# Performance work log

Hardware: AMD Instinct MI355X
Metric: run time of the kernel (lower is better)

## Reference

```python
import jax, jax.numpy as jnp
import numpy as np

D = 768       # model dim
H = 8         # heads
DH = 96       # dim per head
M = 256       # FAVOR+ random features
DEPTH = 6
B = 8
NM = 4        # n_masks
FF = 3072     # 4*dim feedforward
N = 512       # tokens = (1024/16)*(128/16)


def setup_inputs() -> dict:
    key = jax.random.key(0)
    ks = jax.random.split(key, 16)
    g = lambda k, shape: jax.random.normal(k, shape, jnp.float32) * 0.02
    return {
        "mel": jax.random.normal(ks[0], (B, 1, 1024, 128), jnp.float32),
        "patch_w": g(ks[1], (D, 1, 16, 16)),
        "patch_b": jnp.zeros((D,), jnp.float32),
        "pos_embed": g(ks[2], (1, N, D)),
        "proj": jax.random.normal(ks[3], (M, DH), jnp.float32),  # FAVOR+ projection (buffer, no grad)
        "ln1_s": jnp.ones((DEPTH, D)), "ln1_b": jnp.zeros((DEPTH, D)),
        "qkv_w": g(ks[4], (DEPTH, D, 3 * D)), "qkv_b": jnp.zeros((DEPTH, 3 * D)),
        "ao_w": g(ks[5], (DEPTH, D, D)), "ao_b": jnp.zeros((DEPTH, D)),
        "ln2_s": jnp.ones((DEPTH, D)), "ln2_b": jnp.zeros((DEPTH, D)),
        "ff1_w": g(ks[6], (DEPTH, D, FF)), "ff1_b": jnp.zeros((DEPTH, FF)),
        "ff2_w": g(ks[7], (DEPTH, FF, D)), "ff2_b": jnp.zeros((DEPTH, D)),
        "mask_w": g(ks[8], (D, NM)), "mask_b": jnp.zeros((NM,), jnp.float32),
    }


def _ln(x, s, b):
    mu = x.mean(-1, keepdims=True)
    v = ((x - mu) ** 2).mean(-1, keepdims=True)
    return (x - mu) / jnp.sqrt(v + 1e-5) * s + b


def _phi(x, proj, is_query):
    # FAVOR+ softmax-kernel feature map. x: (b,h,n,d), proj: (m,d)
    xd = x * (x.shape[-1] ** -0.25)            # d^{-1/4} data normalizer
    u = jnp.einsum('bhnd,md->bhnm', xd, proj)
    diag = 0.5 * jnp.sum(xd * xd, axis=-1, keepdims=True)
    stab = jnp.max(u, axis=-1, keepdims=True) if is_query else jnp.max(u)
    stab = jax.lax.stop_gradient(stab)          # matches .detach() in performer
    return (jnp.exp(u - diag - stab) + 1e-4) * (proj.shape[0] ** -0.5)


def reference(mel, patch_w, patch_b, pos_embed, proj, ln1_s, ln1_b, qkv_w, qkv_b,
              ao_w, ao_b, ln2_s, ln2_b, ff1_w, ff1_b, ff2_w, ff2_b, mask_w, mask_b):
    # --- frozen AudioMAE patch embed (+pos embed), under no_grad in torch ---
    x = jax.lax.conv_general_dilated(mel, patch_w, (16, 16), 'VALID',
                                     dimension_numbers=('NCHW', 'OIHW', 'NCHW'))  # (B,D,64,8)
    b = x.shape[0]
    x = x.reshape(b, D, -1).transpose(0, 2, 1) + patch_b  # (B,N,D)
    x = x + pos_embed
    x = jax.lax.stop_gradient(x)
    proj = jax.lax.stop_gradient(proj)

    def heads(t):
        return t.reshape(b, -1, H, DH).transpose(0, 2, 1, 3)  # (b,h,n,dh)

    for l in range(DEPTH):
        # --- FAVOR+ linear attention block ---
        h = _ln(x, ln1_s[l], ln1_b[l])
        qkv = h @ qkv_w[l] + qkv_b[l]
        q, k, v = (heads(t) for t in jnp.split(qkv, 3, axis=-1))
        pq = _phi(q, proj, True)
        pk = _phi(k, proj, False)
        ctx = jnp.einsum('bhnm,bhne->bhme', pk, v)       # (b,h,m,dh) linear-time kv summary
        out = jnp.einsum('bhnm,bhme->bhne', pq, ctx)
        den = jnp.einsum('bhnm,bhm->bhn', pq, pk.sum(axis=2))
        out = out / den[..., None]
        out = out.transpose(0, 2, 1, 3).reshape(b, -1, D)
        x = x + out @ ao_w[l] + ao_b[l]
        # --- feedforward block ---
        h = _ln(x, ln2_s[l], ln2_b[l])
        h = jax.nn.gelu(h @ ff1_w[l] + ff1_b[l], approximate=False)
        x = x + h @ ff2_w[l] + ff2_b[l]

    logits = x @ mask_w + mask_b              # (B,N,M)
    masks = jax.nn.sigmoid(logits)
    return masks.transpose(0, 2, 1)           # (B,M,N)
```

## Files before the change

kernel.cpp:

```cpp
#include <hip/hip_runtime.h>
#include <hip/hip_bf16.h>

typedef __bf16 bf16;
typedef __bf16 bf16x8 __attribute__((ext_vector_type(8)));
typedef float f32x4 __attribute__((ext_vector_type(4)));
typedef unsigned int u32;

#define PHI_SCALE  0.31947154f
#define DIAG_SCALE 0.05103104f
#define FEAT_SCALE 0.0625f

__device__ __forceinline__ void glds16(const bf16* g, bf16* l) {
  __builtin_amdgcn_global_load_lds(
      (const __attribute__((address_space(1))) u32*)g,
      (__attribute__((address_space(3))) u32*)l, 16, 0, 0);
}

__device__ __forceinline__ void xcd_remap(int& bx, int& by) {
  int nbx = gridDim.x, nby = gridDim.y;
  int lin = bx + nbx * by;
  int xcd = lin & 7, idx = lin >> 3;
  int mloc = nbx >> 2, nloc = nby >> 1;
  int xm = xcd & 3, xn = xcd >> 2;
  bx = xm * mloc + (idx % mloc);
  by = xn * nloc + (idx / mloc);
}

__device__ __forceinline__ int swz_scol(int lane) {
  return (((lane & 3) ^ ((lane >> 3) & 3)) * 8);
}

__device__ __forceinline__ float waveSum(float v) {
#pragma unroll
  for (int o = 32; o > 0; o >>= 1) v += __shfl_xor(v, o, 64);
  return v;
}
__device__ __forceinline__ float waveMax(float v) {
#pragma unroll
  for (int o = 32; o > 0; o >>= 1) v = fmaxf(v, __shfl_xor(v, o, 64));
  return v;
}
__device__ __forceinline__ float blockSum(float v) {
  __shared__ float tmp[4];
  v = waveSum(v);
  if ((threadIdx.x & 63) == 0) tmp[threadIdx.x >> 6] = v;
  __syncthreads();
  float r = tmp[0] + tmp[1] + tmp[2] + tmp[3];
  __syncthreads();
  return r;
}
__device__ __forceinline__ float blockMax(float v) {
  __shared__ float tmp[4];
  v = waveMax(v);
  if ((threadIdx.x & 63) == 0) tmp[threadIdx.x >> 6] = v;
  __syncthreads();
  float r = fmaxf(fmaxf(tmp[0], tmp[1]), fmaxf(tmp[2], tmp[3]));
  __syncthreads();
  return r;
}

__global__ __launch_bounds__(256) void patches_kernel(const float* __restrict__ mel,
    bf16* __restrict__ patches) {
  int blk = blockIdx.x, t = threadIdx.x;
  int b = blk >> 9, n = blk & 511;
  int r0 = (n >> 3) << 4, c0 = (n & 7) << 4;
  patches[(size_t)blk * 256 + t] =
      (bf16)mel[((size_t)b * 1024 + r0 + (t >> 4)) * 128 + c0 + (t & 15)];
}

__global__ __launch_bounds__(256) void cvt_kernel(const float* __restrict__ src,
    bf16* __restrict__ dst, int n) {
  int i = blockIdx.x * 256 + threadIdx.x;
  if (i < n) dst[i] = (bf16)src[i];
}

__device__ __forceinline__ void tile_transpose(const float* __restrict__ src,
    bf16* __restrict__ dst, int K, int N, int bx, int by) {
  __shared__ float lds[64][65];
  int n0 = bx * 64, k0 = by * 64;
  int t = threadIdx.x;
  for (int idx = t; idx < 4096; idx += 256) {
    int r = idx >> 6, c = idx & 63;
    lds[r][c] = src[(size_t)(k0 + r) * N + n0 + c];
  }
  __syncthreads();
  for (int idx = t; idx < 4096; idx += 256) {
    int r = idx >> 6, c = idx & 63;
    dst[(size_t)(n0 + r) * K + k0 + c] = (bf16)lds[c][r];
  }
}
__global__ __launch_bounds__(256) void transpose4_kernel(
    const float* __restrict__ w0, bf16* __restrict__ d0,
    const float* __restrict__ w1, bf16* __restrict__ d1,
    const float* __restrict__ w2, bf16* __restrict__ d2,
    const float* __restrict__ w3, bf16* __restrict__ d3) {
  int i = blockIdx.x;
  if (i < 432)       { tile_transpose(w0, d0, 768, 2304, i % 36, i / 36); }
  else if (i < 576)  { i -= 432;  tile_transpose(w1, d1, 768, 768, i % 12, i / 12); }
  else if (i < 1152) { i -= 576;  tile_transpose(w2, d2, 768, 3072, i % 48, i / 48);}
  else               { i -= 1152; tile_transpose(w3, d3, 3072, 768, i % 12, i / 12);}
}

__global__ __launch_bounds__(256) void ln_kernel(float* __restrict__ x,
    const float* __restrict__ part,
    const float* __restrict__ s, const float* __restrict__ bta, bf16* __restrict__ h) {
  int row = blockIdx.x;
  float* xr = x + (size_t)row * 768;
  int t = threadIdx.x;
  float v0 = xr[t], v1 = xr[t + 256], v2 = xr[t + 512];
  if (part) {
    const float* p0 = part + (size_t)row * 768;
    const float* p1 = p0 + 4096ull * 768;
    v0 += p0[t]       + p1[t];
    v1 += p0[t + 256] + p1[t + 256];
    v2 += p0[t + 512] + p1[t + 512];
    xr[t] = v0; xr[t + 256] = v1; xr[t + 512] = v2;
  }
  float mu = blockSum(v0 + v1 + v2) * (1.f / 768.f);
  float d0 = v0 - mu, d1 = v1 - mu, d2 = v2 - mu;
  float var = blockSum(d0 * d0 + d1 * d1 + d2 * d2) * (1.f / 768.f);
  float inv = rsqrtf(var + 1e-5f);
  bf16* hr = h + (size_t)row * 768;
  hr[t]       = (bf16)(d0 * inv * s[t]       + bta[t]);
  hr[t + 256] = (bf16)(d1 * inv * s[t + 256] + bta[t + 256]);
  hr[t + 512] = (bf16)(d2 * inv * s[t + 512] + bta[t + 512]);
}

__global__ __launch_bounds__(256) void gemm128(const bf16* __restrict__ A,
    const bf16* __restrict__ B, const float* __restrict__ bias,
    bf16* __restrict__ outb, int N, int K, int mode) {
  __shared__ __attribute__((aligned(16))) bf16 lds_a[2 * 128 * 32];
  __shared__ __attribute__((aligned(16))) bf16 lds_b[2 * 128 * 32];
  int bx = blockIdx.x, by = blockIdx.y;
  xcd_remap(bx, by);
  const int t = threadIdx.x;
  const int m0 = bx * 128, n0 = by * 128;
  const int wave = t >> 6, lane = t & 63;
  const int quad = lane >> 4, id = lane & 15;
  const int wr = wave >> 1, wc = wave & 1;
  const int srow = lane >> 2, scol = swz_scol(lane);
  const bf16* pa0 = A + (size_t)(m0 + wave * 32 + srow) * K + scol;
  const bf16* pa1 = pa0 + (size_t)16 * K;
  const bf16* pb0 = B + (size_t)(n0 + wave * 32 + srow) * K + scol;
  const bf16* pb1 = pb0 + (size_t)16 * K;
  bf16* la = lds_a + wave * 1024;
  bf16* lb = lds_b + wave * 1024;
  const int sl = (quad ^ ((id >> 1) & 3)) * 8;
  f32x4 acc[4][4] = {};
  for (int k0 = 0; k0 < K; k0 += 64) {
    glds16(pa0, la);      glds16(pa1, la + 512);
    glds16(pa0 + 32, la + 4096); glds16(pa1 + 32, la + 4096 + 512);
    glds16(pb0, lb);      glds16(pb1, lb + 512);
    glds16(pb0 + 32, lb + 4096); glds16(pb1 + 32, lb + 4096 + 512);
    pa0 += 64; pa1 += 64; pb0 += 64; pb1 += 64;
    __syncthreads();
#pragma unroll
    for (int kh = 0; kh < 2; kh++) {
      bf16x8 af[4], bg[4];
#pragma unroll
      for (int i = 0; i < 4; i++)
        af[i] = *(bf16x8*)&lds_a[kh * 4096 + (wr * 64 + i * 16 + id) * 32 + sl];
#pragma unroll
      for (int j = 0; j < 4; j++)
        bg[j] = *(bf16x8*)&lds_b[kh * 4096 + (wc * 64 + j * 16 + id) * 32 + sl];
#pragma unroll
      for (int i = 0; i < 4; i++)
#pragma unroll
        for (int j = 0; j < 4; j++)
          acc[i][j] = __builtin_amdgcn_mfma_f32_16x16x32_bf16(af[i], bg[j], acc[i][j], 0, 0, 0);
    }
    __syncthreads();
  }
#pragma unroll
  for (int i = 0; i < 4; i++) {
#pragma unroll
    for (int j = 0; j < 4; j++) {
#pragma unroll
      for (int r = 0; r < 4; r++) {
        int rr = m0 + wr * 64 + i * 16 + quad * 4 + r;
        int cc = n0 + wc * 64 + j * 16 + id;
        float v = acc[i][j][r] + bias[cc];
        if (mode == 1) v = 0.5f * v * (1.0f + erff(v * 0.70710678f));
        outb[(size_t)rr * N + cc] = (bf16)v;
      }
    }
  }
}

__global__ __launch_bounds__(256) void gemm_b64(const bf16* __restrict__ A,
    const bf16* __restrict__ B, const float* __restrict__ bias,
    bf16* __restrict__ outb, float* __restrict__ xout,
    const float* __restrict__ pos, int N, int kchunk, int mode) {
  __shared__ __attribute__((aligned(16))) bf16 lds_a[2 * 128 * 32];
  __shared__ __attribute__((aligned(16))) bf16 lds_b[2 * 64 * 32];
  int bx = blockIdx.x, by = blockIdx.y;
  xcd_remap(bx, by);
  const int t = threadIdx.x;
  const int m0 = bx * 128, n0 = by * 64;
  const int kz = blockIdx.z;
  const int k_start = kz * kchunk;
  const int wave = t >> 6, lane = t & 63;
  const int quad = lane >> 4, id = lane & 15;
  const int srow = lane >> 2, scol = swz_scol(lane);
  const int K = kchunk * gridDim.z;
  const size_t slice = (size_t)kz * gridDim.x * 128 * N;
  const bf16* pa0 = A + (size_t)(m0 + wave * 32 + srow) * K + k_start + scol;
  const bf16* pa1 = pa0 + (size_t)16 * K;
  const bf16* pb  = B + (size_t)(n0 + wave * 16 + srow) * K + k_start + scol;
  bf16* la = lds_a + wave * 1024;
  bf16* lb = lds_b + wave * 512;
  const int sl = (quad ^ ((id >> 1) & 3)) * 8;
  f32x4 acc[2][4] = {};
  for (int k0 = 0; k0 < kchunk; k0 += 64) {
    glds16(pa0, la);      glds16(pa1, la + 512);
    glds16(pa0 + 32, la + 4096); glds16(pa1 + 32, la + 4096 + 512);
    glds16(pb, lb);       glds16(pb + 32, lb + 2048);
    pa0 += 64; pa1 += 64; pb += 64;
    __syncthreads();
#pragma unroll
    for (int kh = 0; kh < 2; kh++) {
      bf16x8 af[2], bg[4];
#pragma unroll
      for (int i = 0; i < 2; i++)
        af[i] = *(bf16x8*)&lds_a[kh * 4096 + (wave * 32 + i * 16 + id) * 32 + sl];
#pragma unroll
      for (int j = 0; j < 4; j++)
        bg[j] = *(bf16x8*)&lds_b[kh * 2048 + (j * 16 + id) * 32 + sl];
#pragma unroll
      for (int i = 0; i < 2; i++)
#pragma unroll
        for (int j = 0; j < 4; j++)
          acc[i][j] = __builtin_amdgcn_mfma_f32_16x16x32_bf16(af[i], bg[j], acc[i][j], 0, 0, 0);
    }
    __syncthreads();
  }
#pragma unroll
  for (int i = 0; i < 2; i++) {
#pragma unroll
    for (int j = 0; j < 4; j++) {
#pragma unroll
      for (int r = 0; r < 4; r++) {
        int rr = m0 + wave * 32 + i * 16 + quad * 4 + r;
        int cc = n0 + j * 16 + id;
        if (mode == 4) {
          float v = acc[i][j][r] + (kz == 0 ? bias[cc] : 0.f);
          xout[slice + (size_t)rr * N + cc] = v;
        } else {
          float v = acc[i][j][r] + bias[cc];
          if (mode == 0) {
            outb[(size_t)rr * N + cc] = (bf16)v;
          } else if (mode == 1) {
            outb[(size_t)rr * N + cc] = (bf16)(0.5f * v * (1.0f + erff(v * 0.70710678f)));
          } else {
            xout[(size_t)rr * N + cc] = v + pos[(size_t)(rr & 511) * 768 + cc];
          }
        }
      }
    }
  }
}

__global__ __launch_bounds__(256) void phi_q_kernel(const bf16* __restrict__ qkv,
    const bf16* __restrict__ proj, bf16* __restrict__ pq) {
  __shared__ __attribute__((aligned(16))) bf16 lA[3][64 * 32];
  __shared__ __attribute__((aligned(16))) bf16 lB[3][256 * 32];
  __shared__ float sqlds[64];
  const int t = threadIdx.x;
  const int nt = blockIdx.x, bh = blockIdx.y;
  const int b = bh >> 3, h = bh & 7;
  const int n0 = nt * 64;
  const bf16* Abase = qkv + ((size_t)(b * 512 + n0)) * 2304 + h * 96;
#pragma unroll
  for (int c = 0; c < 3; c++) {
    int v = c * 256 + t;
    int row = v / 12, s = v % 12;
    *(bf16x8*)&lA[s >> 2][row * 32 + (s & 3) * 8] = *(const bf16x8*)&Abase[(size_t)row * 2304 + s * 8];
  }
#pragma unroll
  for (int c = 0; c < 12; c++) {
    int v = c * 256 + t;
    int row = v / 12, s = v % 12;
    *(bf16x8*)&lB[s >> 2][row * 32 + (s & 3) * 8] = *(const bf16x8*)&proj[(size_t)row * 96 + s * 8];
  }
  __syncthreads();
  const int wave = t >> 6, lane = t & 63, quad = lane >> 4, id = lane & 15;
  f32x4 acc[16] = {};
  float sq = 0.f;
#pragma unroll
  for (int kb = 0; kb < 3; kb++) {
    bf16x8 af = *(bf16x8*)&lA[kb][(wave * 16 + id) * 32 + quad * 8];
#pragma unroll
    for (int e = 0; e < 8; e++) { float fv = (float)af[e]; sq += fv * fv; }
#pragma unroll
    for (int j = 0; j < 16; j++) {
      bf16x8 bg = *(bf16x8*)&lB[kb][(j * 16 + id) * 32 + quad * 8];
      acc[j] = __builtin_amdgcn_mfma_f32_16x16x32_bf16(af, bg, acc[j], 0, 0, 0);
    }
  }
  sq += __shfl_xor(sq, 16, 64);
  sq += __shfl_xor(sq, 32, 64);
  if (quad == 0) sqlds[wave * 16 + id] = sq;
  __syncthreads();
#pragma unroll
  for (int r = 0; r < 4; r++) {
    int rrow = quad * 4 + r;
    float dg = DIAG_SCALE * sqlds[wave * 16 + rrow];
    float mx = -1e30f;
#pragma unroll
    for (int j = 0; j < 16; j++) mx = fmaxf(mx, acc[j][r]);
    mx = fmaxf(mx, __shfl_xor(mx, 1, 64));
    mx = fmaxf(mx, __shfl_xor(mx, 2, 64));
    mx = fmaxf(mx, __shfl_xor(mx, 4, 64));
    mx = fmaxf(mx, __shfl_xor(mx, 8, 64));
    float umax = mx * PHI_SCALE;
#pragma unroll
    for (int j = 0; j < 16; j++) {
      float uu = acc[j][r] * PHI_SCALE;
      float val = (expf(uu - dg - umax) + 1e-4f) * FEAT_SCALE;
      pq[((size_t)bh * 512 + n0 + wave * 16 + rrow) * 256 + j * 16 + id] = (bf16)val;
    }
  }
}

__global__ __launch_bounds__(256) void phi_k_kernel(const bf16* __restrict__ qkv,
    const bf16* __restrict__ proj, bf16* __restrict__ pkT, float* __restrict__ kbm) {
  __shared__ __attribute__((aligned(16))) bf16 lA[3][64 * 32];
  __shared__ __attribute__((aligned(16))) bf16 lB[3][256 * 32];
  __shared__ float sqlds[64];
  __shared__ float bmax4[4];
  const int t = threadIdx.x;
  const int nt = blockIdx.x, bh = blockIdx.y;
  const int b = bh >> 3, h = bh & 7;
  const int n0 = nt * 64;
  const bf16* Abase = qkv + ((size_t)(b * 512 + n0)) * 2304 + 768 + h * 96;
#pragma unroll
  for (int c = 0; c < 3; c++) {
    int v = c * 256 + t;
    int row = v / 12, s = v % 12;
    *(bf16x8*)&lA[s >> 2][row * 32 + (s & 3) * 8] = *(const bf16x8*)&Abase[(size_t)row * 2304 + s * 8];
  }
#pragma unroll
  for (int c = 0; c < 12; c++) {
    int v = c * 256 + t;
    int row = v / 12, s = v % 12;
    *(bf16x8*)&lB[s >> 2][row * 32 + (s & 3) * 8] = *(const bf16x8*)&proj[(size_t)row * 96 + s * 8];
  }
  __syncthreads();
  const int wave = t >> 6, lane = t & 63, quad = lane >> 4, id = lane & 15;
  f32x4 acc[16] = {};
  float sq = 0.f;
#pragma unroll
  for (int kb = 0; kb < 3; kb++) {
    bf16x8 af = *(bf16x8*)&lA[kb][(wave * 16 + id) * 32 + quad * 8];
#pragma unroll
    for (int e = 0; e < 8; e++) { float fv = (float)af[e]; sq += fv * fv; }
#pragma unroll
    for (int j = 0; j < 16; j++) {
      bf16x8 bg = *(bf16x8*)&lB[kb][(j * 16 + id) * 32 + quad * 8];
      acc[j] = __builtin_amdgcn_mfma_f32_16x16x32_bf16(af, bg, acc[j], 0, 0, 0);
    }
  }
  sq += __shfl_xor(sq, 16, 64);
  sq += __shfl_xor(sq, 32, 64);
  if (quad == 0) sqlds[wave * 16 + id] = sq;
  float bm = -1e30f;
#pragma unroll
  for (int j = 0; j < 16; j++)
#pragma unroll
    for (int r = 0; r < 4; r++) bm = fmaxf(bm, acc[j][r]);
  bm = waveMax(bm);
  if (lane == 0) bmax4[wave] = bm;
  __syncthreads();
  float blkmax = fmaxf(fmaxf(bmax4[0], bmax4[1]), fmaxf(bmax4[2], bmax4[3])) * PHI_SCALE;
  if (t == 0) kbm[bh * 8 + nt] = blkmax;
  bf16* sT = &lB[0][0];
#pragma unroll
  for (int r = 0; r < 4; r++) {
    int rrow = wave * 16 + quad * 4 + r;
    float dg = DIAG_SCALE * sqlds[rrow];
#pragma unroll
    for (int j = 0; j < 16; j++) {
      float uu = acc[j][r] * PHI_SCALE;
      sT[(j * 16 + id) * 66 + rrow] = (bf16)expf(uu - dg - blkmax);
    }
  }
  __syncthreads();
  bf16* dst = pkT + ((size_t)bh * 256) * 512 + n0;
#pragma unroll
  for (int it = 0; it < 64; it++) {
    int idx = it * 256 + t;
    int m = idx >> 6, n = idx & 63;
    dst[(size_t)m * 512 + n] = sT[m * 66 + n];
  }
}

__global__ __launch_bounds__(256) void vt_kernel(const bf16* __restrict__ qkv, bf16* __restrict__ vT) {
  __shared__ bf16 lds[64][97];
  int bh = blockIdx.y, b = bh >> 3, h = bh & 7;
  int n0 = blockIdx.x * 64;
  int t = threadIdx.x;
  const bf16* src = qkv + ((size_t)b * 512 + n0) * 2304 + 1536 + h * 96;
  for (int idx = t; idx < 6144; idx += 256) {
    int r = idx / 96, c = idx % 96;
    lds[r][c] = src[(size_t)r * 2304 + c];
  }
  __syncthreads();
  bf16* dst = vT + (size_t)bh * 96 * 512 + n0;
  for (int idx = t; idx < 6144; idx += 256) {
    int e = idx >> 6, nn = idx & 63;
    dst[(size_t)e * 512 + nn] = lds[nn][e];
  }
}

__global__ __launch_bounds__(256) void ctx_gemm(const bf16* __restrict__ pkT,
    const bf16* __restrict__ vT, const float* __restrict__ kbm,
    bf16* __restrict__ ctxT, float* __restrict__ ksum) {
  __shared__ __attribute__((aligned(16))) bf16 lds_a[64 * 40];
  __shared__ __attribute__((aligned(16))) bf16 lds_b[96 * 40];
  const int t = threadIdx.x;
  const int bh = blockIdx.y, m0 = blockIdx.x * 64;
  const bf16* A = pkT + (size_t)bh * 256 * 512;
  const bf16* B = vT + (size_t)bh * 96 * 512;
  const int wave = t >> 6, lane = t & 63;
  const int quad = lane >> 4, id = lane & 15;
  const int row = t >> 2, kof = (t & 3) * 8;
  float gm = blockMax(fmaxf(kbm[t], kbm[t + 256]));
  f32x4 acc[6] = {};
  float ks = 0.f;
  const float offc = 1e-4f * FEAT_SCALE;
  for (int k0 = 0; k0 < 512; k0 += 32) {
    float fs = expf(kbm[bh * 8 + (k0 >> 6)] - gm) * FEAT_SCALE;
    *(bf16x8*)&lds_a[row * 40 + kof] = *(const bf16x8*)&A[(size_t)(m0 + row) * 512 + k0 + kof];
    for (int idx = t; idx < 384; idx += 256) {
      int r2 = idx >> 2, k2 = (idx & 3) * 8;
      *(bf16x8*)&lds_b[r2 * 40 + k2] = *(const bf16x8*)&B[(size_t)r2 * 512 + k0 + k2];
    }
    __syncthreads();
    bf16x8 af = *(bf16x8*)&lds_a[(wave * 16 + id) * 40 + quad * 8];
    bf16x8 afs;
#pragma unroll
    for (int e = 0; e < 8; e++) {
      float f = (float)af[e] * fs + offc;
      ks += f;
      afs[e] = (bf16)f;
    }
#pragma unroll
    for (int j = 0; j < 6; j++) {
      bf16x8 bg = *(bf16x8*)&lds_b[(j * 16 + id) * 40 + quad * 8];
      acc[j] = __builtin_amdgcn_mfma_f32_16x16x32_bf16(afs, bg, acc[j], 0, 0, 0);
    }
    __syncthreads();
  }
  ks += __shfl_xor(ks, 16, 64);
  ks += __shfl_xor(ks, 32, 64);
  if (quad == 0) ksum[bh * 256 + m0 + wave * 16 + id] = ks;
#pragma unroll
  for (int j = 0; j < 6; j++)
#pragma unroll
    for (int r = 0; r < 4; r++) {
      int e = j * 16 + id;
      int m = m0 + wave * 16 + quad * 4 + r;
      ctxT[((size_t)bh * 96 + e) * 256 + m] = (bf16)acc[j][r];
    }
}

__global__ __launch_bounds__(256) void out_gemm(const bf16* __restrict__ pq,
    const bf16* __restrict__ ctxT, const float* __restrict__ ksum, bf16* __restrict__ attn) {
  __shared__ __attribute__((aligned(16))) bf16 lds_a[64 * 40];
  __shared__ __attribute__((aligned(16))) bf16 lds_b[96 * 40];
  __shared__ float den_lds[64];
  const int t = threadIdx.x;
  const int bh = blockIdx.y, m0 = blockIdx.x * 64;
  const int b = bh >> 3, h = bh & 7;
  const bf16* A = pq + (size_t)bh * 512 * 256;
  const bf16* B = ctxT + (size_t)bh * 96 * 256;
  const int wave = t >> 6, lane = t & 63;
  const int quad = lane >> 4, id = lane & 15;
  const int row = t >> 2, kof = (t & 3) * 8;
  f32x4 acc[6] = {};
  float den = 0.f;
  for (int k0 = 0; k0 < 256; k0 += 32) {
    *(bf16x8*)&lds_a[row * 40 + kof] = *(const bf16x8*)&A[(size_t)(m0 + row) * 256 + k0 + kof];
    for (int idx = t; idx < 384; idx += 256) {
      int r2 = idx >> 2, k2 = (idx & 3) * 8;
      *(bf16x8*)&lds_b[r2 * 40 + k2] = *(const bf16x8*)&B[(size_t)r2 * 256 + k0 + k2];
    }
    __syncthreads();
    bf16x8 af = *(bf16x8*)&lds_a[(wave * 16 + id) * 40 + quad * 8];
    const f32x4* kp = (const f32x4*)(ksum + bh * 256 + k0 + quad * 8);
    f32x4 k0v = kp[0], k1v = kp[1];
#pragma unroll
    for (int e = 0; e < 4; e++) den += (float)af[e] * k0v[e];
#pragma unroll
    for (int e = 0; e < 4; e++) den += (float)af[e + 4] * k1v[e];
#pragma unroll
    for (int j = 0; j < 6; j++) {
      bf16x8 bg = *(bf16x8*)&lds_b[(j * 16 + id) * 40 + quad * 8];
      acc[j] = __builtin_amdgcn_mfma_f32_16x16x32_bf16(af, bg, acc[j], 0, 0, 0);
    }
    __syncthreads();
  }
  den += __shfl_xor(den, 16, 64);
  den += __shfl_xor(den, 32, 64);
  if (quad == 0) den_lds[wave * 16 + id] = den;
  __syncthreads();
#pragma unroll
  for (int j = 0; j < 6; j++)
#pragma unroll
    for (int r = 0; r < 4; r++) {
      int e = j * 16 + id;
      int n = m0 + wave * 16 + quad * 4 + r;
      float v = acc[j][r] / fmaxf(den_lds[wave * 16 + quad * 4 + r], 1e-30f);
      attn[((size_t)(b * 512 + n)) * 768 + h * 96 + e] = (bf16)v;
    }
}

__global__ __launch_bounds__(256) void mask_kernel(const float* __restrict__ x,
    const float* __restrict__ part,
    const float* __restrict__ mw, const float* __restrict__ mb, float* __restrict__ out) {
  int row = blockIdx.x * 4 + (threadIdx.x >> 6);
  int lane = threadIdx.x & 63;
  int b = row >> 9, n = row & 511;
  const float* xr = x + (size_t)row * 768;
  const float* p0 = part + (size_t)row * 768;
  const float* p1 = p0 + 4096ull * 768;
  float a0 = 0, a1 = 0, a2 = 0, a3 = 0;
  for (int d = lane; d < 768; d += 64) {
    float xv = xr[d] + p0[d] + p1[d];
    a0 += xv * mw[d * 4 + 0];
    a1 += xv * mw[d * 4 + 1];
    a2 += xv * mw[d * 4 + 2];
    a3 += xv * mw[d * 4 + 3];
  }
  a0 = waveSum(a0); a1 = waveSum(a1); a2 = waveSum(a2); a3 = waveSum(a3);
  if (lane == 0) {
    out[((size_t)b * 4 + 0) * 512 + n] = 1.f / (1.f + expf(-(a0 + mb[0])));
    out[((size_t)b * 4 + 1) * 512 + n] = 1.f / (1.f + expf(-(a1 + mb[1])));
    out[((size_t)b * 4 + 2) * 512 + n] = 1.f / (1.f + expf(-(a2 + mb[2])));
    out[((size_t)b * 4 + 3) * 512 + n] = 1.f / (1.f + expf(-(a3 + mb[3])));
  }
}

extern "C" void kernel_launch(void* const* d_in, const int* in_sizes, int n_in,
                              void* d_out, int out_size, void* d_ws, size_t ws_size,
                              hipStream_t stream) {
  const float* mel     = (const float*)d_in[0];
  const float* patch_w = (const float*)d_in[1];
  const float* patch_b = (const float*)d_in[2];
  const float* pos     = (const float*)d_in[3];
  const float* proj    = (const float*)d_in[4];
  const float* ln1_s   = (const float*)d_in[5];
  const float* ln1_b   = (const float*)d_in[6];
  const float* qkv_w   = (const float*)d_in[7];
  const float* qkv_b   = (const float*)d_in[8];
  const float* ao_w    = (const float*)d_in[9];
  const float* ao_b    = (const float*)d_in[10];
  const float* ln2_s   = (const float*)d_in[11];
  const float* ln2_b   = (const float*)d_in[12];
  const float* ff1_w   = (const float*)d_in[13];
  const float* ff1_b   = (const float*)d_in[14];
  const float* ff2_w   = (const float*)d_in[15];
  const float* ff2_b   = (const float*)d_in[16];
  const float* mask_w  = (const float*)d_in[17];
  const float* mask_b  = (const float*)d_in[18];

  char* ws = (char*)d_ws;
  size_t off = 0;
  auto alloc = [&](size_t bytes) { void* p = ws + off; off += (bytes + 255) & ~(size_t)255; return p; };
  float* x     = (float*)alloc(4096ull * 768 * 4);
  float* xpart = (float*)alloc(2ull * 4096 * 768 * 4);
  bf16* h      = (bf16*)alloc(4096ull * 768 * 2);
  bf16* qkv    = (bf16*)alloc(4096ull * 2304 * 2);
  bf16* wtq    = (bf16*)alloc(2304ull * 768 * 2);
  bf16* wta    = (bf16*)alloc(768ull * 768 * 2);
  bf16* wtf1   = (bf16*)alloc(3072ull * 768 * 2);
  bf16* wtf2   = (bf16*)alloc(768ull * 3072 * 2);
  bf16* patches= (bf16*)alloc(4096ull * 256 * 2);
  bf16* pwb    = (bf16*)alloc(768ull * 256 * 2);
  bf16* projb  = (bf16*)alloc(256ull * 96 * 2);
  bf16* pq     = (bf16*)alloc(8388608ull * 2);
  bf16* pkT    = (bf16*)alloc(8388608ull * 2);
  bf16* vT     = (bf16*)alloc(64ull * 96 * 512 * 2);
  bf16* ctxT   = (bf16*)alloc(64ull * 96 * 256 * 2);
  float* ksum  = (float*)alloc(64ull * 256 * 4);
  float* kbm   = (float*)alloc(512ull * 4);
  bf16* attn   = (bf16*)alloc(4096ull * 768 * 2);
  bf16* ffh    = (bf16*)alloc(4096ull * 3072 * 2);
  if (ws_size < off) return;

  patches_kernel<<<4096, 256, 0, stream>>>(mel, patches);
  cvt_kernel<<<768, 256, 0, stream>>>(patch_w, pwb, 196608);
  cvt_kernel<<<96, 256, 0, stream>>>(proj, projb, 24576);
  gemm_b64<<<dim3(32, 12), 256, 0, stream>>>(patches, pwb, patch_b, nullptr, x, pos,
                                             768, 256, 3);

  for (int l = 0; l < 6; l++) {
    transpose4_kernel<<<1728, 256, 0, stream>>>(
        qkv_w + (size_t)l * 768 * 2304, wtq,
        ao_w + (size_t)l * 768 * 768, wta,
        ff1_w + (size_t)l * 768 * 3072, wtf1,
        ff2_w + (size_t)l * 3072 * 768, wtf2);

    ln_kernel<<<4096, 256, 0, stream>>>(x, l == 0 ? nullptr : xpart,
                                        ln1_s + l * 768, ln1_b + l * 768, h);
    gemm128<<<dim3(32, 18), 256, 0, stream>>>(h, wtq, qkv_b + l * 2304, qkv, 2304, 768, 0);

    phi_q_kernel<<<dim3(8, 64), 256, 0, stream>>>(qkv, projb, pq);
    phi_k_kernel<<<dim3(8, 64), 256, 0, stream>>>(qkv, projb, pkT, kbm);
    vt_kernel<<<dim3(8, 64), 256, 0, stream>>>(qkv, vT);
    ctx_gemm<<<dim3(4, 64), 256, 0, stream>>>(pkT, vT, kbm, ctxT, ksum);
    out_gemm<<<dim3(8, 64), 256, 0, stream>>>(pq, ctxT, ksum, attn);
    gemm_b64<<<dim3(32, 12, 2), 256, 0, stream>>>(attn, wta, ao_b + l * 768, nullptr, xpart,
                                                  nullptr, 768, 384, 4);

    ln_kernel<<<4096, 256, 0, stream>>>(x, xpart, ln2_s + l * 768, ln2_b + l * 768, h);
    gemm128<<<dim3(32, 24), 256, 0, stream>>>(h, wtf1, ff1_b + l * 3072, ffh, 3072, 768, 1);
    gemm_b64<<<dim3(32, 12, 2), 256, 0, stream>>>(ffh, wtf2, ff2_b + l * 768, nullptr, xpart,
                                                  nullptr, 768, 1536, 4);
  }

  mask_kernel<<<1024, 256, 0, stream>>>(x, xpart, mask_w, mask_b, (float*)d_out);
}
```

Measured before the change: 1.376 ms.

## Fuse phi_q, phi_k and V transpose into one kernel; load A fragments directly

```diff
diff --git a/kernel.cpp b/kernel.cpp
--- a/kernel.cpp
+++ b/kernel.cpp
@@ -260,162 +260,130 @@
   }
 }
 
-__global__ __launch_bounds__(256) void phi_q_kernel(const bf16* __restrict__ qkv,
-    const bf16* __restrict__ proj, bf16* __restrict__ pq) {
-  __shared__ __attribute__((aligned(16))) bf16 lA[3][64 * 32];
-  __shared__ __attribute__((aligned(16))) bf16 lB[3][256 * 32];
-  __shared__ float sqlds[64];
-  const int t = threadIdx.x;
-  const int nt = blockIdx.x, bh = blockIdx.y;
-  const int b = bh >> 3, h = bh & 7;
-  const int n0 = nt * 64;
-  const bf16* Abase = qkv + ((size_t)(b * 512 + n0)) * 2304 + h * 96;
-#pragma unroll
-  for (int c = 0; c < 3; c++) {
-    int v = c * 256 + t;
-    int row = v / 12, s = v % 12;
-    *(bf16x8*)&lA[s >> 2][row * 32 + (s & 3) * 8] = *(const bf16x8*)&Abase[(size_t)row * 2304 + s * 8];
-  }
-#pragma unroll
-  for (int c = 0; c < 12; c++) {
-    int v = c * 256 + t;
-    int row = v / 12, s = v % 12;
-    *(bf16x8*)&lB[s >> 2][row * 32 + (s & 3) * 8] = *(const bf16x8*)&proj[(size_t)row * 96 + s * 8];
-  }
-  __syncthreads();
-  const int wave = t >> 6, lane = t & 63, quad = lane >> 4, id = lane & 15;
-  f32x4 acc[16] = {};
-  float sq = 0.f;
-#pragma unroll
-  for (int kb = 0; kb < 3; kb++) {
-    bf16x8 af = *(bf16x8*)&lA[kb][(wave * 16 + id) * 32 + quad * 8];
-#pragma unroll
-    for (int e = 0; e < 8; e++) { float fv = (float)af[e]; sq += fv * fv; }
-#pragma unroll
-    for (int j = 0; j < 16; j++) {
-      bf16x8 bg = *(bf16x8*)&lB[kb][(j * 16 + id) * 32 + quad * 8];
-      acc[j] = __builtin_amdgcn_mfma_f32_16x16x32_bf16(af, bg, acc[j], 0, 0, 0);
-    }
-  }
-  sq += __shfl_xor(sq, 16, 64);
-  sq += __shfl_xor(sq, 32, 64);
-  if (quad == 0) sqlds[wave * 16 + id] = sq;
-  __syncthreads();
-#pragma unroll
-  for (int r = 0; r < 4; r++) {
-    int rrow = quad * 4 + r;
-    float dg = DIAG_SCALE * sqlds[wave * 16 + rrow];
-    float mx = -1e30f;
-#pragma unroll
-    for (int j = 0; j < 16; j++) mx = fmaxf(mx, acc[j][r]);
-    mx = fmaxf(mx, __shfl_xor(mx, 1, 64));
-    mx = fmaxf(mx, __shfl_xor(mx, 2, 64));
-    mx = fmaxf(mx, __shfl_xor(mx, 4, 64));
-    mx = fmaxf(mx, __shfl_xor(mx, 8, 64));
-    float umax = mx * PHI_SCALE;
-#pragma unroll
-    for (int j = 0; j < 16; j++) {
-      float uu = acc[j][r] * PHI_SCALE;
-      float val = (expf(uu - dg - umax) + 1e-4f) * FEAT_SCALE;
-      pq[((size_t)bh * 512 + n0 + wave * 16 + rrow) * 256 + j * 16 + id] = (bf16)val;
-    }
-  }
-}
-
-__global__ __launch_bounds__(256) void phi_k_kernel(const bf16* __restrict__ qkv,
-    const bf16* __restrict__ proj, bf16* __restrict__ pkT, float* __restrict__ kbm) {
-  __shared__ __attribute__((aligned(16))) bf16 lA[3][64 * 32];
-  __shared__ __attribute__((aligned(16))) bf16 lB[3][256 * 32];
+__global__ __launch_bounds__(256) void phi_fused(const bf16* __restrict__ qkv,
+    const bf16* __restrict__ proj, bf16* __restrict__ pq,
+    bf16* __restrict__ pkT, float* __restrict__ kbm, bf16* __restrict__ vT) {
+  __shared__ __attribute__((aligned(16))) bf16 smem[3 * 256 * 32];
   __shared__ float sqlds[64];
   __shared__ float bmax4[4];
   const int t = threadIdx.x;
   const int nt = blockIdx.x, bh = blockIdx.y;
   const int b = bh >> 3, h = bh & 7;
   const int n0 = nt * 64;
-  const bf16* Abase = qkv + ((size_t)(b * 512 + n0)) * 2304 + 768 + h * 96;
-#pragma unroll
-  for (int c = 0; c < 3; c++) {
-    int v = c * 256 + t;
-    int row = v / 12, s = v % 12;
-    *(bf16x8*)&lA[s >> 2][row * 32 + (s & 3) * 8] = *(const bf16x8*)&Abase[(size_t)row * 2304 + s * 8];
-  }
 #pragma unroll
   for (int c = 0; c < 12; c++) {
     int v = c * 256 + t;
     int row = v / 12, s = v % 12;
-    *(bf16x8*)&lB[s >> 2][row * 32 + (s & 3) * 8] = *(const bf16x8*)&proj[(size_t)row * 96 + s * 8];
+    *(bf16x8*)&smem[(s >> 2) * 8192 + row * 32 + (s & 3) * 8] =
+        *(const bf16x8*)&proj[(size_t)row * 96 + s * 8];
   }
   __syncthreads();
   const int wave = t >> 6, lane = t & 63, quad = lane >> 4, id = lane & 15;
-  f32x4 acc[16] = {};
-  float sq = 0.f;
-#pragma unroll
-  for (int kb = 0; kb < 3; kb++) {
-    bf16x8 af = *(bf16x8*)&lA[kb][(wave * 16 + id) * 32 + quad * 8];
-#pragma unroll
-    for (int e = 0; e < 8; e++) { float fv = (float)af[e]; sq += fv * fv; }
-#pragma unroll
-    for (int j = 0; j < 16; j++) {
-      bf16x8 bg = *(bf16x8*)&lB[kb][(j * 16 + id) * 32 + quad * 8];
-      acc[j] = __builtin_amdgcn_mfma_f32_16x16x32_bf16(af, bg, acc[j], 0, 0, 0);
-    }
-  }
-  sq += __shfl_xor(sq, 16, 64);
-  sq += __shfl_xor(sq, 32, 64);
-  if (quad == 0) sqlds[wave * 16 + id] = sq;
-  float bm = -1e30f;
-#pragma unroll
-  for (int j = 0; j < 16; j++)
-#pragma unroll
-    for (int r = 0; r < 4; r++) bm = fmaxf(bm, acc[j][r]);
-  bm = waveMax(bm);
-  if (lane == 0) bmax4[wave] = bm;
-  __syncthreads();
-  float blkmax = fmaxf(fmaxf(bmax4[0], bmax4[1]), fmaxf(bmax4[2], bmax4[3])) * PHI_SCALE;
-  if (t == 0) kbm[bh * 8 + nt] = blkmax;
-  bf16* sT = &lB[0][0];
-#pragma unroll
-  for (int r = 0; r < 4; r++) {
-    int rrow = wave * 16 + quad * 4 + r;
-    float dg = DIAG_SCALE * sqlds[rrow];
-#pragma unroll
-    for (int j = 0; j < 16; j++) {
-      float uu = acc[j][r] * PHI_SCALE;
-      sT[(j * 16 + id) * 66 + rrow] = (bf16)expf(uu - dg - blkmax);
-    }
-  }
-  __syncthreads();
-  bf16* dst = pkT + ((size_t)bh * 256) * 512 + n0;
-#pragma unroll
-  for (int it = 0; it < 64; it++) {
-    int idx = it * 256 + t;
-    int m = idx >> 6, n = idx & 63;
-    dst[(size_t)m * 512 + n] = sT[m * 66 + n];
-  }
-}
-
-__global__ __launch_bounds__(256) void vt_kernel(const bf16* __restrict__ qkv, bf16* __restrict__ vT) {
-  __shared__ bf16 lds[64][97];
-  int bh = blockIdx.y, b = bh >> 3, h = bh & 7;
-  int n0 = blockIdx.x * 64;
-  int t = threadIdx.x;
-  const bf16* src = qkv + ((size_t)b * 512 + n0) * 2304 + 1536 + h * 96;
-  for (int idx = t; idx < 6144; idx += 256) {
-    int r = idx / 96, c = idx % 96;
-    lds[r][c] = src[(size_t)r * 2304 + c];
-  }
-  __syncthreads();
-  bf16* dst = vT + (size_t)bh * 96 * 512 + n0;
-  for (int idx = t; idx < 6144; idx += 256) {
-    int e = idx >> 6, nn = idx & 63;
-    dst[(size_t)e * 512 + nn] = lds[nn][e];
+  const bf16* qrow = qkv + ((size_t)(b * 512 + n0 + wave * 16 + id)) * 2304 + h * 96;
+
+  {
+    f32x4 acc[16] = {};
+    float sq = 0.f;
+#pragma unroll
+    for (int kb = 0; kb < 3; kb++) {
+      bf16x8 af = *(const bf16x8*)&qrow[kb * 32 + quad * 8];
+#pragma unroll
+      for (int e = 0; e < 8; e++) { float fv = (float)af[e]; sq += fv * fv; }
+#pragma unroll
+      for (int j = 0; j < 16; j++) {
+        bf16x8 bg = *(bf16x8*)&smem[kb * 8192 + (j * 16 + id) * 32 + quad * 8];
+        acc[j] = __builtin_amdgcn_mfma_f32_16x16x32_bf16(af, bg, acc[j], 0, 0, 0);
+      }
+    }
+    sq += __shfl_xor(sq, 16, 64);
+    sq += __shfl_xor(sq, 32, 64);
+    if (quad == 0) sqlds[wave * 16 + id] = sq;
+    __syncthreads();
+#pragma unroll
+    for (int r = 0; r < 4; r++) {
+      int rrow = quad * 4 + r;
+      float dg = DIAG_SCALE * sqlds[wave * 16 + rrow];
+      float mx = -1e30f;
+#pragma unroll
+      for (int j = 0; j < 16; j++) mx = fmaxf(mx, acc[j][r]);
+      mx = fmaxf(mx, __shfl_xor(mx, 1, 64));
+      mx = fmaxf(mx, __shfl_xor(mx, 2, 64));
+      mx = fmaxf(mx, __shfl_xor(mx, 4, 64));
+      mx = fmaxf(mx, __shfl_xor(mx, 8, 64));
+      float umax = mx * PHI_SCALE;
+#pragma unroll
+      for (int j = 0; j < 16; j++) {
+        float uu = acc[j][r] * PHI_SCALE;
+        float val = (expf(uu - dg - umax) + 1e-4f) * FEAT_SCALE;
+        pq[((size_t)bh * 512 + n0 + wave * 16 + rrow) * 256 + j * 16 + id] = (bf16)val;
+      }
+    }
+  }
+  __syncthreads();
+
+  {
+    f32x4 acc[16] = {};
+    float sq = 0.f;
+#pragma unroll
+    for (int kb = 0; kb < 3; kb++) {
+      bf16x8 af = *(const bf16x8*)&qrow[768 + kb * 32 + quad * 8];
+#pragma unroll
+      for (int e = 0; e < 8; e++) { float fv = (float)af[e]; sq += fv * fv; }
+#pragma unroll
+      for (int j = 0; j < 16; j++) {
+        bf16x8 bg = *(bf16x8*)&smem[kb * 8192 + (j * 16 + id) * 32 + quad * 8];
+        acc[j] = __builtin_amdgcn_mfma_f32_16x16x32_bf16(af, bg, acc[j], 0, 0, 0);
+      }
+    }
+    sq += __shfl_xor(sq, 16, 64);
+    sq += __shfl_xor(sq, 32, 64);
+    if (quad == 0) sqlds[wave * 16 + id] = sq;
+    float bm = -1e30f;
+#pragma unroll
+    for (int j = 0; j < 16; j++)
+#pragma unroll
+      for (int r = 0; r < 4; r++) bm = fmaxf(bm, acc[j][r]);
+    bm = waveMax(bm);
+    if (lane == 0) bmax4[wave] = bm;
+    __syncthreads();
+    float blkmax = fmaxf(fmaxf(bmax4[0], bmax4[1]), fmaxf(bmax4[2], bmax4[3])) * PHI_SCALE;
+    if (t == 0) kbm[bh * 8 + nt] = blkmax;
+    bf16* sT = smem;
+    bf16* vlds = smem + 16896;
+#pragma unroll
+    for (int r = 0; r < 4; r++) {
+      int rrow = wave * 16 + quad * 4 + r;
+      float dg = DIAG_SCALE * sqlds[rrow];
+#pragma unroll
+      for (int j = 0; j < 16; j++) {
+        float uu = acc[j][r] * PHI_SCALE;
+        sT[(j * 16 + id) * 66 + rrow] = (bf16)expf(uu - dg - blkmax);
+      }
+    }
+    const bf16* vsrc = qkv + ((size_t)(b * 512 + n0)) * 2304 + 1536 + h * 96;
+    for (int idx = t; idx < 6144; idx += 256) {
+      int r = idx / 96, c = idx % 96;
+      vlds[r * 97 + c] = vsrc[(size_t)r * 2304 + c];
+    }
+    __syncthreads();
+    bf16* dst = pkT + ((size_t)bh * 256) * 512 + n0;
+#pragma unroll
+    for (int it = 0; it < 64; it++) {
+      int idx = it * 256 + t;
+      int m = idx >> 6, n = idx & 63;
+      dst[(size_t)m * 512 + n] = sT[m * 66 + n];
+    }
+    bf16* vdst = vT + (size_t)bh * 96 * 512 + n0;
+    for (int idx = t; idx < 6144; idx += 256) {
+      int e = idx >> 6, nn = idx & 63;
+      vdst[(size_t)e * 512 + nn] = vlds[nn * 97 + e];
+    }
   }
 }
 
 __global__ __launch_bounds__(256) void ctx_gemm(const bf16* __restrict__ pkT,
     const bf16* __restrict__ vT, const float* __restrict__ kbm,
     bf16* __restrict__ ctxT, float* __restrict__ ksum) {
-  __shared__ __attribute__((aligned(16))) bf16 lds_a[64 * 40];
   __shared__ __attribute__((aligned(16))) bf16 lds_b[96 * 40];
   const int t = threadIdx.x;
   const int bh = blockIdx.y, m0 = blockIdx.x * 64;
@@ -423,20 +391,19 @@
   const bf16* B = vT + (size_t)bh * 96 * 512;
   const int wave = t >> 6, lane = t & 63;
   const int quad = lane >> 4, id = lane & 15;
-  const int row = t >> 2, kof = (t & 3) * 8;
   float gm = blockMax(fmaxf(kbm[t], kbm[t + 256]));
   f32x4 acc[6] = {};
   float ks = 0.f;
   const float offc = 1e-4f * FEAT_SCALE;
+  const bf16* arow = A + (size_t)(m0 + wave * 16 + id) * 512 + quad * 8;
   for (int k0 = 0; k0 < 512; k0 += 32) {
     float fs = expf(kbm[bh * 8 + (k0 >> 6)] - gm) * FEAT_SCALE;
-    *(bf16x8*)&lds_a[row * 40 + kof] = *(const bf16x8*)&A[(size_t)(m0 + row) * 512 + k0 + kof];
     for (int idx = t; idx < 384; idx += 256) {
       int r2 = idx >> 2, k2 = (idx & 3) * 8;
       *(bf16x8*)&lds_b[r2 * 40 + k2] = *(const bf16x8*)&B[(size_t)r2 * 512 + k0 + k2];
     }
-    __syncthreads();
-    bf16x8 af = *(bf16x8*)&lds_a[(wave * 16 + id) * 40 + quad * 8];
+    bf16x8 af = *(const bf16x8*)&arow[k0];
+    __syncthreads();
     bf16x8 afs;
 #pragma unroll
     for (int e = 0; e < 8; e++) {
@@ -466,7 +433,6 @@
 
 __global__ __launch_bounds__(256) void out_gemm(const bf16* __restrict__ pq,
     const bf16* __restrict__ ctxT, const float* __restrict__ ksum, bf16* __restrict__ attn) {
-  __shared__ __attribute__((aligned(16))) bf16 lds_a[64 * 40];
   __shared__ __attribute__((aligned(16))) bf16 lds_b[96 * 40];
   __shared__ float den_lds[64];
   const int t = threadIdx.x;
@@ -476,17 +442,16 @@
   const bf16* B = ctxT + (size_t)bh * 96 * 256;
   const int wave = t >> 6, lane = t & 63;
   const int quad = lane >> 4, id = lane & 15;
-  const int row = t >> 2, kof = (t & 3) * 8;
   f32x4 acc[6] = {};
   float den = 0.f;
+  const bf16* arow = A + (size_t)(m0 + wave * 16 + id) * 256 + quad * 8;
   for (int k0 = 0; k0 < 256; k0 += 32) {
-    *(bf16x8*)&lds_a[row * 40 + kof] = *(const bf16x8*)&A[(size_t)(m0 + row) * 256 + k0 + kof];
     for (int idx = t; idx < 384; idx += 256) {
       int r2 = idx >> 2, k2 = (idx & 3) * 8;
       *(bf16x8*)&lds_b[r2 * 40 + k2] = *(const bf16x8*)&B[(size_t)r2 * 256 + k0 + k2];
     }
-    __syncthreads();
-    bf16x8 af = *(bf16x8*)&lds_a[(wave * 16 + id) * 40 + quad * 8];
+    bf16x8 af = *(const bf16x8*)&arow[k0];
+    __syncthreads();
     const f32x4* kp = (const f32x4*)(ksum + bh * 256 + k0 + quad * 8);
     f32x4 k0v = kp[0], k1v = kp[1];
 #pragma unroll
@@ -605,9 +570,7 @@
                                         ln1_s + l * 768, ln1_b + l * 768, h);
     gemm128<<<dim3(32, 18), 256, 0, stream>>>(h, wtq, qkv_b + l * 2304, qkv, 2304, 768, 0);
 
-    phi_q_kernel<<<dim3(8, 64), 256, 0, stream>>>(qkv, projb, pq);
-    phi_k_kernel<<<dim3(8, 64), 256, 0, stream>>>(qkv, projb, pkT, kbm);
-    vt_kernel<<<dim3(8, 64), 256, 0, stream>>>(qkv, vT);
+    phi_fused<<<dim3(8, 64), 256, 0, stream>>>(qkv, projb, pq, pkT, kbm, vT);
     ctx_gemm<<<dim3(4, 64), 256, 0, stream>>>(pkT, vT, kbm, ctxT, ksum);
     out_gemm<<<dim3(8, 64), 256, 0, stream>>>(pq, ctxT, ksum, attn);
     gemm_b64<<<dim3(32, 12, 2), 256, 0, stream>>>(attn, wta, ao_b + l * 768, nullptr, xpart,
```

Measured after the change: 1.323 ms. -3.9%, faster.
